# Kernel optimization log

Measured on AMD Instinct MI355X. Metric: run time of the kernel, lower is better.

Reference implementation:

```python
import jax, jax.numpy as jnp
import numpy as np

NLAYERS = 8
NSUB = 4
L = NLAYERS * NSUB
DMIN, DMAX = 2.0, 20.0
SIGMOID_OFFSET = -1.0
H, W = 960, 1920
N_RAYS = 131072


def _grid_sample(img, grid):
    """torch.F.grid_sample equivalent: bilinear, align_corners=True, zeros padding.
    img: (B, C, H, W); grid: (B, Hg, Wg, 2) with grid[...,0]=x (width), grid[...,1]=y (height).
    Returns (B, C, Hg, Wg)."""
    B, C, Hh, Ww = img.shape
    x = (grid[..., 0] + 1.0) * 0.5 * (Ww - 1)
    y = (grid[..., 1] + 1.0) * 0.5 * (Hh - 1)
    x0 = jnp.floor(x)
    y0 = jnp.floor(y)
    x1 = x0 + 1.0
    y1 = y0 + 1.0
    wx1 = x - x0
    wy1 = y - y0
    bidx = jnp.arange(B)[:, None, None]

    def corner(iy, ix, w):
        valid = (ix >= 0) & (ix <= Ww - 1) & (iy >= 0) & (iy <= Hh - 1)
        iyc = jnp.clip(iy, 0, Hh - 1).astype(jnp.int32)
        ixc = jnp.clip(ix, 0, Ww - 1).astype(jnp.int32)
        v = img[bidx, :, iyc, ixc]  # (B, Hg, Wg, C)
        return jnp.where(valid[..., None], v, 0.0) * w[..., None]

    out = (corner(y0, x0, (1.0 - wy1) * (1.0 - wx1))
           + corner(y0, x1, (1.0 - wy1) * wx1)
           + corner(y1, x0, wy1 * (1.0 - wx1))
           + corner(y1, x1, wy1 * wx1))
    return jnp.moveaxis(out, -1, 1)


def setup_inputs() -> dict:
    key = jax.random.key(0)
    k1, k2, k3, k4 = jax.random.split(key, 4)
    origins = jax.random.uniform(k1, (N_RAYS, 3), jnp.float32)          # |O| < dmin -> valid intersections
    directions = jax.random.normal(k2, (N_RAYS, 3), jnp.float32)
    alpha = jax.random.uniform(k3, (L, 1, H, W), jnp.float32, -1.0, 1.0)
    rgb = jax.random.uniform(k4, (NLAYERS, 3, H, W), jnp.float32, -1.0, 1.0)
    pose = jnp.eye(4, dtype=jnp.float32)
    planes = jnp.asarray(1.0 / np.linspace(1.0 / DMIN, 1.0 / DMAX, L), jnp.float32)
    return {"origins": origins, "directions": directions, "pose": pose,
            "alpha": alpha, "rgb": rgb, "planes": planes}


def reference(origins, directions, pose, alpha, rgb, planes):
    center = pose[:3, 3]                                   # (3,)
    O = origins[:, None, :]                                # (N,1,3)
    D = directions[:, None, :]                             # (N,1,3)
    ray = O - center
    a = jnp.sum(D * D, axis=-1)                            # (N,1)
    b = 2.0 * jnp.sum(D * ray, axis=-1)                    # (N,1)
    c = jnp.sum(ray * ray, axis=-1) - planes[None, :] ** 2  # (N,L)
    disc = b * b - 4.0 * a * c
    sq = jnp.sqrt(disc)
    t0 = (-b + sq) / (2.0 * a)                             # (N,L)
    t1 = (-b - sq) / (2.0 * a)
    mask = (t0 * t1) < 0.0                                 # (N,L)
    inter = O + D * t0[:, :, None]                         # (N,L,3)

    xyz = inter - center
    xyzn = xyz / planes.reshape(1, -1, 1)                  # on unit sphere per layer
    uvs = jnp.stack([xyzn[..., 2],
                     jnp.arctan2(xyzn[..., 1], -xyzn[..., 0]) / jnp.pi], axis=2)  # (N,L,2)
    uvs = jnp.transpose(uvs, (1, 0, 2))[:, None]           # (L,1,N,2)

    alphas = _grid_sample(alpha, uvs)                      # (L,1,1,N)
    a_sig = jax.nn.sigmoid(alphas - SIGMOID_OFFSET)
    a_sig = jnp.transpose(a_sig, (0, 2, 3, 1))             # (L,1,N,1)
    m = jnp.transpose(mask, (1, 0))[:, None, :, None]      # (L,1,N,1)
    a_sig = jnp.where(m, a_sig, 0.0)

    rgbs = jax.nn.sigmoid(_grid_sample(rgb, uvs[::NSUB]))  # (nlayers,3,1,N)
    rgbs = jnp.transpose(rgbs, (0, 1, 3, 2))               # (nlayers,3,N,1)
    rgbs = jnp.repeat(rgbs, NSUB, axis=0)                  # (L,3,N,1)

    trans = jnp.cumprod(1.0 - a_sig, axis=0)
    excl = jnp.concatenate([jnp.ones_like(trans[:1]), trans[:-1]], axis=0)  # exclusive cumprod
    weight = excl * a_sig                                  # (L,1,N,1)
    out = jnp.sum(weight * rgbs, axis=0, keepdims=True)    # (1,3,N,1)
    return out
```

## Files before the change

kernel.cpp:

```cpp
#include <hip/hip_runtime.h>
#include <math.h>

namespace {
constexpr int kNRays = 131072;
constexpr int kNL = 8;
constexpr int kSub = 4;
constexpr int kH = 960;
constexpr int kW = 1920;
constexpr int kHW = kH * kW;
constexpr int kGridB = 64;
constexpr int kNBuckets = kGridB * kGridB;
constexpr int kKeyPlane = 20;

__device__ __forceinline__ float sigmoidf(float z) {
    return 1.0f / (1.0f + __expf(-z));
}

__device__ __forceinline__ unsigned morton2(unsigned x, unsigned y) {
    unsigned r = 0;
    #pragma unroll
    for (int i = 0; i < 6; ++i) {
        r |= ((x >> i) & 1u) << (2 * i);
        r |= ((y >> i) & 1u) << (2 * i + 1);
    }
    return r;
}

__device__ __forceinline__ void ray_uv(float rx, float ry, float rz,
                                       float dx, float dy, float dz,
                                       float p, float& gx, float& gy) {
    float a  = dx*dx + dy*dy + dz*dz;
    float b  = 2.0f * (dx*rx + dy*ry + dz*rz);
    float rr = rx*rx + ry*ry + rz*rz;
    float c = rr - p * p;
    float disc = b * b - 4.0f * a * c;
    float sq = sqrtf(fmaxf(disc, 0.0f));
    float t0 = (-b + sq) / (2.0f * a);
    float hx = rx + dx * t0;
    float hy = ry + dy * t0;
    float hz = rz + dz * t0;
    float invp = 1.0f / p;
    float xn = hx * invp, yn = hy * invp, zn = hz * invp;
    gx = zn;
    gy = atan2f(yn, -xn) * 0.31830988618379067f;
}

__device__ __forceinline__ void bilin_setup(float gx, float gy, int idx[4], float w[4]) {
    float x = (gx + 1.0f) * (0.5f * (float)(kW - 1));
    float y = (gy + 1.0f) * (0.5f * (float)(kH - 1));
    float x0f = floorf(x), y0f = floorf(y);
    float wx1 = x - x0f, wy1 = y - y0f;
    float wx0 = 1.0f - wx1, wy0 = 1.0f - wy1;
    bool vx0 = (x0f >= 0.0f) && (x0f <= (float)(kW - 1));
    bool vx1 = (x0f + 1.0f >= 0.0f) && (x0f + 1.0f <= (float)(kW - 1));
    bool vy0 = (y0f >= 0.0f) && (y0f <= (float)(kH - 1));
    bool vy1 = (y0f + 1.0f >= 0.0f) && (y0f + 1.0f <= (float)(kH - 1));
    int x0 = min(max((int)x0f, 0), kW - 1);
    int x1 = min(max((int)x0f + 1, 0), kW - 1);
    int y0 = min(max((int)y0f, 0), kH - 1);
    int y1 = min(max((int)y0f + 1, 0), kH - 1);
    idx[0] = y0 * kW + x0; w[0] = (vy0 && vx0) ? wy0 * wx0 : 0.0f;
    idx[1] = y0 * kW + x1; w[1] = (vy0 && vx1) ? wy0 * wx1 : 0.0f;
    idx[2] = y1 * kW + x0; w[2] = (vy1 && vx0) ? wy1 * wx0 : 0.0f;
    idx[3] = y1 * kW + x1; w[3] = (vy1 && vx1) ? wy1 * wx1 : 0.0f;
}
}

__global__ __launch_bounds__(256) void key_hist_kernel(
    const float* __restrict__ origins, const float* __restrict__ dirs,
    const float* __restrict__ pose, const float* __restrict__ planes,
    unsigned* __restrict__ keys, unsigned* __restrict__ hist)
{
    int i = blockIdx.x * blockDim.x + threadIdx.x;
    if (i >= kNRays) return;
    float cx = pose[3], cy = pose[7], cz = pose[11];
    float rx = origins[3*i+0] - cx, ry = origins[3*i+1] - cy, rz = origins[3*i+2] - cz;
    float dx = dirs[3*i+0], dy = dirs[3*i+1], dz = dirs[3*i+2];
    float gx, gy;
    ray_uv(rx, ry, rz, dx, dy, dz, planes[kKeyPlane], gx, gy);
    int qu = min(max((int)((gx * 0.5f + 0.5f) * (float)kGridB), 0), kGridB - 1);
    int qv = min(max((int)((gy * 0.5f + 0.5f) * (float)kGridB), 0), kGridB - 1);
    unsigned k = morton2((unsigned)qu, (unsigned)qv);
    keys[i] = k;
    atomicAdd(&hist[k], 1u);
}

__global__ __launch_bounds__(256) void scan_kernel(unsigned* __restrict__ hist)
{
    __shared__ unsigned part[256];
    int t = threadIdx.x;
    unsigned loc[kNBuckets / 256];
    unsigned sum = 0;
    #pragma unroll
    for (int j = 0; j < kNBuckets / 256; ++j) {
        loc[j] = hist[t * (kNBuckets / 256) + j];
        sum += loc[j];
    }
    part[t] = sum;
    __syncthreads();
    for (int off = 1; off < 256; off <<= 1) {
        unsigned v = (t >= off) ? part[t - off] : 0u;
        __syncthreads();
        part[t] += v;
        __syncthreads();
    }
    unsigned prefix = part[t] - sum;
    #pragma unroll
    for (int j = 0; j < kNBuckets / 256; ++j) {
        unsigned v = loc[j];
        hist[t * (kNBuckets / 256) + j] = prefix;
        prefix += v;
    }
}

__global__ __launch_bounds__(256) void scatter_kernel(
    const unsigned* __restrict__ keys, unsigned* __restrict__ offs,
    unsigned* __restrict__ perm)
{
    int i = blockIdx.x * blockDim.x + threadIdx.x;
    if (i >= kNRays) return;
    unsigned pos = atomicAdd(&offs[keys[i]], 1u);
    perm[pos] = (unsigned)i;
}

__global__ __launch_bounds__(256) void msi_field_kernel(
    const float* __restrict__ origins,
    const float* __restrict__ dirs,
    const float* __restrict__ pose,
    const float* __restrict__ alpha,
    const float* __restrict__ rgb,
    const float* __restrict__ planes,
    const unsigned* __restrict__ perm,
    float* __restrict__ out)
{
    int slot = blockIdx.x * blockDim.x + threadIdx.x;
    if (slot >= kNRays) return;
    int i = (int)perm[slot];

    float cx = pose[3], cy = pose[7], cz = pose[11];
    float ox = origins[3*i+0], oy = origins[3*i+1], oz = origins[3*i+2];
    float dx = dirs[3*i+0],    dy = dirs[3*i+1],    dz = dirs[3*i+2];

    float rx = ox - cx, ry = oy - cy, rz = oz - cz;
    float a  = dx*dx + dy*dy + dz*dz;
    float b  = 2.0f * (dx*rx + dy*ry + dz*rz);
    float rr = rx*rx + ry*ry + rz*rz;
    float inv2a = 1.0f / (2.0f * a);

    float T = 1.0f;
    float accR = 0.0f, accG = 0.0f, accB = 0.0f;
    float sr = 0.0f, sg = 0.0f, sb = 0.0f;

    for (int nl = 0; nl < kNL; ++nl) {
        #pragma unroll
        for (int s = 0; s < kSub; ++s) {
            const int l = nl * kSub + s;
            float p = planes[l];
            float c = rr - p * p;
            float disc = b * b - 4.0f * a * c;
            float sq = sqrtf(disc);
            float t0 = (-b + sq) * inv2a;
            float t1 = (-b - sq) * inv2a;
            bool mask = (t0 * t1) < 0.0f;

            float hx = rx + dx * t0;
            float hy = ry + dy * t0;
            float hz = rz + dz * t0;
            float invp = 1.0f / p;
            float xn = hx * invp, yn = hy * invp, zn = hz * invp;

            float gx = zn;
            float gy = atan2f(yn, -xn) * 0.31830988618379067f;

            int idx[4]; float w[4];
            bilin_setup(gx, gy, idx, w);

            const float* aimg = alpha + (size_t)l * kHW;
            float av = w[0]*aimg[idx[0]] + w[1]*aimg[idx[1]]
                     + w[2]*aimg[idx[2]] + w[3]*aimg[idx[3]];
            float asig = mask ? sigmoidf(av + 1.0f) : 0.0f;

            if (s == 0) {
                const float* rimg = rgb + (size_t)nl * 3 * kHW;
                const float* gimg = rimg + kHW;
                const float* bimg = rimg + 2 * kHW;
                float rv = w[0]*rimg[idx[0]] + w[1]*rimg[idx[1]]
                         + w[2]*rimg[idx[2]] + w[3]*rimg[idx[3]];
                float gv = w[0]*gimg[idx[0]] + w[1]*gimg[idx[1]]
                         + w[2]*gimg[idx[2]] + w[3]*gimg[idx[3]];
                float bv = w[0]*bimg[idx[0]] + w[1]*bimg[idx[1]]
                         + w[2]*bimg[idx[2]] + w[3]*bimg[idx[3]];
                sr = sigmoidf(rv); sg = sigmoidf(gv); sb = sigmoidf(bv);
            }

            float wt = T * asig;
            accR += wt * sr;
            accG += wt * sg;
            accB += wt * sb;
            T *= (1.0f - asig);
        }
    }

    out[i]            = accR;
    out[kNRays + i]   = accG;
    out[2*kNRays + i] = accB;
}

extern "C" void kernel_launch(void* const* d_in, const int* in_sizes, int n_in,
                              void* d_out, int out_size, void* d_ws, size_t ws_size,
                              hipStream_t stream) {
    const float* origins = (const float*)d_in[0];
    const float* dirs    = (const float*)d_in[1];
    const float* pose    = (const float*)d_in[2];
    const float* alpha   = (const float*)d_in[3];
    const float* rgb     = (const float*)d_in[4];
    const float* planes  = (const float*)d_in[5];
    float* out = (float*)d_out;

    unsigned* hist = (unsigned*)d_ws;
    unsigned* keys = hist + kNBuckets;
    unsigned* perm = keys + kNRays;

    hipMemsetAsync(hist, 0, kNBuckets * sizeof(unsigned), stream);

    dim3 block(256);
    dim3 gridR((kNRays + 255) / 256);
    hipLaunchKernelGGL(key_hist_kernel, gridR, block, 0, stream,
                       origins, dirs, pose, planes, keys, hist);
    hipLaunchKernelGGL(scan_kernel, dim3(1), block, 0, stream, hist);
    hipLaunchKernelGGL(scatter_kernel, gridR, block, 0, stream, keys, hist, perm);
    hipLaunchKernelGGL(msi_field_kernel, gridR, block, 0, stream,
                       origins, dirs, pose, alpha, rgb, planes, perm, out);
}
```

Before: 495.5 us.

## Split each ray's layers across four lanes and combine with shuffle compositing

The main kernel now assigns four threads per ray, each compositing two of the eight layer groups, so there are four times as many threads. Partial transmittance and colour are merged with an associative over-operator through xor shuffles, and lane 0 writes the result. Launch bounds now request higher occupancy. This raises memory-level parallelism for the gather-bound sampling. The cost is redundant per-ray setup in every lane and some shuffle overhead.

Measured after the change: 586.6 us. 1.18x slower.

```diff
diff --git a/kernel.cpp b/kernel.cpp
--- a/kernel.cpp
+++ b/kernel.cpp
@@ -3,7 +3,8 @@
 
 namespace {
 constexpr int kNRays = 131072;
-constexpr int kNL = 8;
+constexpr int kLanesPerRay = 4;
+constexpr int kGroupsPerLane = 2;
 constexpr int kSub = 4;
 constexpr int kH = 960;
 constexpr int kW = 1920;
@@ -123,7 +124,7 @@
     perm[pos] = (unsigned)i;
 }
 
-__global__ __launch_bounds__(256) void msi_field_kernel(
+__global__ __launch_bounds__(256, 8) void msi_field_kernel(
     const float* __restrict__ origins,
     const float* __restrict__ dirs,
     const float* __restrict__ pose,
@@ -133,7 +134,9 @@
     const unsigned* __restrict__ perm,
     float* __restrict__ out)
 {
-    int slot = blockIdx.x * blockDim.x + threadIdx.x;
+    int tid = blockIdx.x * blockDim.x + threadIdx.x;
+    int slot = tid / kLanesPerRay;
+    int r = tid & (kLanesPerRay - 1);
     if (slot >= kNRays) return;
     int i = (int)perm[slot];
 
@@ -151,7 +154,9 @@
     float accR = 0.0f, accG = 0.0f, accB = 0.0f;
     float sr = 0.0f, sg = 0.0f, sb = 0.0f;
 
-    for (int nl = 0; nl < kNL; ++nl) {
+    #pragma unroll
+    for (int g = 0; g < kGroupsPerLane; ++g) {
+        const int nl = r * kGroupsPerLane + g;
         #pragma unroll
         for (int s = 0; s < kSub; ++s) {
             const int l = nl * kSub + s;
@@ -201,9 +206,26 @@
         }
     }
 
-    out[i]            = accR;
-    out[kNRays + i]   = accG;
-    out[2*kNRays + i] = accB;
+    #pragma unroll
+    for (int m = 1; m <= 2; m <<= 1) {
+        float pT = __shfl_xor(T,    m);
+        float pR = __shfl_xor(accR, m);
+        float pG = __shfl_xor(accG, m);
+        float pB = __shfl_xor(accB, m);
+        if ((r & m) == 0) {
+            accR += T * pR; accG += T * pG; accB += T * pB;
+            T *= pT;
+        } else {
+            accR = pR + pT * accR; accG = pG + pT * accG; accB = pB + pT * accB;
+            T = pT * T;
+        }
+    }
+
+    if (r == 0) {
+        out[i]            = accR;
+        out[kNRays + i]   = accG;
+        out[2*kNRays + i] = accB;
+    }
 }
 
 extern "C" void kernel_launch(void* const* d_in, const int* in_sizes, int n_in,
@@ -229,6 +251,9 @@
                        origins, dirs, pose, planes, keys, hist);
     hipLaunchKernelGGL(scan_kernel, dim3(1), block, 0, stream, hist);
     hipLaunchKernelGGL(scatter_kernel, gridR, block, 0, stream, keys, hist, perm);
-    hipLaunchKernelGGL(msi_field_kernel, gridR, block, 0, stream,
+
+    const int total = kNRays * kLanesPerRay;
+    dim3 gridM((total + 255) / 256);
+    hipLaunchKernelGGL(msi_field_kernel, gridM, block, 0, stream,
                        origins, dirs, pose, alpha, rgb, planes, perm, out);
 }
```
